# Kernel tuning notes

Measured on AMD Instinct MI355X. Metric: run time of the kernel, lower is better.

Reference implementation:

```python
import jax, jax.numpy as jnp
import numpy as np

GROUP_SIZE = 32
PACKED_SIZE = GROUP_SIZE * 3 // 8  # 12
OUT_FEATURES = 4096
IN_FEATURES = 4096

# Precomputed static unpack constants per position i in [0, 32)
_I = np.arange(GROUP_SIZE)
_BYTE_IDX = (_I * 3) // 8                     # which byte holds the low bits
_BIT_OFF = (_I * 3) % 8                       # bit offset inside that byte
_LOW_MASK = np.where(_BIT_OFF <= 5, 7, (1 << (8 - _BIT_OFF)) - 1)
_HIGH_MASK = np.where(_BIT_OFF <= 5, 0, (1 << np.maximum(_BIT_OFF - 5, 0)) - 1)
_HIGH_SHIFT = np.where(_BIT_OFF <= 5, 0, 8 - _BIT_OFF)
_BYTE_IDX_NEXT = np.minimum(_BYTE_IDX + 1, PACKED_SIZE - 1)


def block_dequantize_3bit(packed, normalization):
    """packed: [G, 12] int (uint8 values), normalization: [G, 1] -> [G*32] f32."""
    p = packed.astype(jnp.int32)
    norm = normalization.astype(jnp.float32)
    b0 = p[:, _BYTE_IDX]        # [G, 32]
    b1 = p[:, _BYTE_IDX_NEXT]   # [G, 32]
    shift = jnp.asarray(_BIT_OFF, jnp.int32)
    low = (b0 >> shift) & jnp.asarray(_LOW_MASK, jnp.int32)
    high = (b1 & jnp.asarray(_HIGH_MASK, jnp.int32)) << jnp.asarray(_HIGH_SHIFT, jnp.int32)
    x_quant = (low | high).astype(jnp.float32)  # values in [0, 7]
    x_norm = x_quant / 7.0
    x = x_norm * 2.0 * norm - norm              # [G, 32]
    return x.reshape(-1)


def setup_inputs() -> dict:
    key = jax.random.key(0)
    k1, k2, k3, k4 = jax.random.split(key, 4)
    num_groups = OUT_FEATURES * IN_FEATURES // GROUP_SIZE
    x = jax.random.normal(k1, (8192, IN_FEATURES), dtype=jnp.float32)
    weight_q3 = jax.random.randint(k2, (num_groups, PACKED_SIZE), 0, 256, dtype=jnp.int32).astype(jnp.uint8)
    weight_norm = (jax.random.uniform(k3, (num_groups, 1), dtype=jnp.float32) * 0.99 + 0.01).astype(jnp.float16)
    bias = (jax.random.normal(k4, (OUT_FEATURES,), dtype=jnp.float32) * 0.02).astype(jnp.float16)
    return {"x": x, "weight_q3": weight_q3, "weight_norm": weight_norm, "bias": bias}


def reference(x, weight_q3, weight_norm, bias):
    w_flat = block_dequantize_3bit(weight_q3, weight_norm)          # f32 [out*in]
    w = w_flat.reshape(OUT_FEATURES, IN_FEATURES).astype(jnp.float16)
    x_half = x.astype(jnp.float16)
    result = jnp.dot(x_half, w.T) + bias                             # [N, out] fp16
    return result.astype(x.dtype)
```

## Files before the change

kernel.cpp:

```cpp
#include <hip/hip_runtime.h>
#include <hip/hip_fp16.h>
#include <stdint.h>

#define IN_F   4096
#define OUT_F  4096
#define M_ROWS 8192

typedef _Float16 v8h __attribute__((ext_vector_type(8)));
typedef float    v4f __attribute__((ext_vector_type(4)));

__global__ void __launch_bounds__(256)
dequant_kernel(const int* __restrict__ q, const float* __restrict__ norm,
               _Float16* __restrict__ w) {
    int g = blockIdx.x * blockDim.x + threadIdx.x;
    const int4* p = (const int4*)(q + (size_t)g * 12);
    int4 q0 = p[0], q1 = p[1], q2 = p[2];
    uint32_t b[12] = {(uint32_t)q0.x, (uint32_t)q0.y, (uint32_t)q0.z, (uint32_t)q0.w,
                      (uint32_t)q1.x, (uint32_t)q1.y, (uint32_t)q1.z, (uint32_t)q1.w,
                      (uint32_t)q2.x, (uint32_t)q2.y, (uint32_t)q2.z, (uint32_t)q2.w};
    uint64_t lo = 0, hi = 0;
#pragma unroll
    for (int i = 0; i < 8; ++i) lo |= (uint64_t)(b[i] & 0xff) << (8 * i);
#pragma unroll
    for (int i = 0; i < 8; ++i) hi |= (uint64_t)(b[4 + i] & 0xff) << (8 * i);
    float nrm = norm[g];
    float scale = nrm * (2.0f / 7.0f);
    v8h out[4];
#pragma unroll
    for (int i = 0; i < 32; ++i) {
        int p3 = 3 * i;
        uint32_t qv = (i <= 20) ? (uint32_t)((lo >> p3) & 7)
                                : (uint32_t)((hi >> (p3 - 32)) & 7);
        float v = fmaf((float)qv, scale, -nrm);
        out[i >> 3][i & 7] = (_Float16)v;
    }
    v8h* dst = (v8h*)(w + (size_t)g * 32);
    dst[0] = out[0]; dst[1] = out[1]; dst[2] = out[2]; dst[3] = out[3];
}

__global__ void __launch_bounds__(256)
castx_kernel(const float* __restrict__ x, _Float16* __restrict__ o) {
    size_t i = ((size_t)blockIdx.x * blockDim.x + threadIdx.x) * 8;
    float4 a = *(const float4*)(x + i);
    float4 b = *(const float4*)(x + i + 4);
    v8h r;
    r[0] = (_Float16)a.x; r[1] = (_Float16)a.y; r[2] = (_Float16)a.z; r[3] = (_Float16)a.w;
    r[4] = (_Float16)b.x; r[5] = (_Float16)b.y; r[6] = (_Float16)b.z; r[7] = (_Float16)b.w;
    *(v8h*)(o + i) = r;
}

#define KU 32

__global__ void __launch_bounds__(512, 2)
gemm_kernel(const _Float16* __restrict__ A,
            const _Float16* __restrict__ B,
            const float* __restrict__ bias,
            float* __restrict__ C) {
    __shared__ __align__(16) char smem[131072];

    int pid = blockIdx.x;
    int c  = pid & 7;
    int s  = pid >> 3;
    int pm = ((c & 3) << 3) | (s & 7);
    int pn = ((c >> 2) << 3) | (s >> 3);
    const int m0 = pm * 256, n0 = pn * 256;

    int t = threadIdx.x;
    int lane = t & 63, wid = t >> 6;
    int wm = wid >> 2, wn = wid & 3;
    int lr = lane & 15, qd = lane >> 4;

    int chr  = (((lane & 1) << 2) | qd) ^ ((lr >> 1) & 7);
    int aoff = wm * 8192 + (lr >> 1) * 128 + chr * 16;
    int boff = 16384 + wn * 4096 + (lr >> 1) * 128 + chr * 16;

    int line = t >> 3, chl = t & 7;
    int chd  = chl ^ (line & 7);
    int rr0  = 2 * line + (chd >> 2);
    int cc0  = chd & 3;
    const _Float16* gA0 = A + (size_t)(m0 + rr0) * IN_F + cc0 * 8;
    const _Float16* gA1 = gA0 + (size_t)128 * IN_F;
    const _Float16* gB0 = B + (size_t)(n0 + rr0) * IN_F + cc0 * 8;
    const _Float16* gB1 = gB0 + (size_t)128 * IN_F;
    const int dA = t * 16;
    const int dB = 16384 + t * 16;

    v4f acc[8][4] = {};
    v8h fa0[8], fb0[4], fa1[8], fb1[4];

#define STAGE4(SL2)                                                                 \
    do {                                                                            \
        char* db_ = smem + (SL2) * 32768;                                           \
        __builtin_amdgcn_global_load_lds(                                           \
            (const __attribute__((address_space(1))) void*)gA0,                     \
            (__attribute__((address_space(3))) void*)(db_ + dA), 16, 0, 0);         \
        __builtin_amdgcn_global_load_lds(                                           \
            (const __attribute__((address_space(1))) void*)gA1,                     \
            (__attribute__((address_space(3))) void*)(db_ + dA + 8192), 16, 0, 0);  \
        __builtin_amdgcn_global_load_lds(                                           \
            (const __attribute__((address_space(1))) void*)gB0,                     \
            (__attribute__((address_space(3))) void*)(db_ + dB), 16, 0, 0);         \
        __builtin_amdgcn_global_load_lds(                                           \
            (const __attribute__((address_space(1))) void*)gB1,                     \
            (__attribute__((address_space(3))) void*)(db_ + dB + 8192), 16, 0, 0);  \
    } while (0)

#define READFRAG(SLOT, FA, FB)                                                      \
    do {                                                                            \
        const char* sp_ = smem + (SLOT) * 32768;                                    \
        _Pragma("unroll") for (int i = 0; i < 8; ++i)                               \
            FA[i] = *(const v8h*)(sp_ + aoff + i * 1024);                           \
        _Pragma("unroll") for (int j = 0; j < 4; ++j)                               \
            FB[j] = *(const v8h*)(sp_ + boff + j * 1024);                           \
    } while (0)

#define STEP(SL, FCA, FCB, FNA, FNB, DO_STAGE, DO_PREF, VM)                         \
    do {                                                                            \
        asm volatile("" ::: "memory");      \
        if (DO_PREF) READFRAG(((SL) + 1) & 3, FNA, FNB);                            \
        if (DO_STAGE) {                                                             \
            STAGE4(((SL) + 3) & 3);                                                 \
            gA0 += KU; gA1 += KU; gB0 += KU; gB1 += KU;                             \
        }                                                                           \
        __builtin_amdgcn_s_setprio(1);                                              \
        _Pragma("unroll") for (int i = 0; i < 8; ++i)                               \
            _Pragma("unroll") for (int j = 0; j < 4; ++j)                           \
                acc[i][j] = __builtin_amdgcn_mfma_f32_16x16x32_f16(                 \
                    FCA[i], FCB[j], acc[i][j], 0, 0, 0);                            \
        __builtin_amdgcn_s_setprio(0);                                              \
        asm volatile("s_waitcnt vmcnt(" #VM ")" ::: "memory");                      \
        __builtin_amdgcn_s_barrier();                                               \
    } while (0)

    STAGE4(0); gA0 += KU; gA1 += KU; gB0 += KU; gB1 += KU;
    STAGE4(1); gA0 += KU; gA1 += KU; gB0 += KU; gB1 += KU;
    STAGE4(2); gA0 += KU; gA1 += KU; gB0 += KU; gB1 += KU;
    asm volatile("s_waitcnt vmcnt(4)" ::: "memory");
    __builtin_amdgcn_s_barrier();
    asm volatile("" ::: "memory");
    READFRAG(0, fa0, fb0);

#pragma unroll 1
    for (int b4 = 0; b4 < 31; ++b4) {
        STEP(0, fa0, fb0, fa1, fb1, 1, 1, 4);
        STEP(1, fa1, fb1, fa0, fb0, 1, 1, 4);
        STEP(2, fa0, fb0, fa1, fb1, 1, 1, 4);
        STEP(3, fa1, fb1, fa0, fb0, 1, 1, 4);
    }
    STEP(0, fa0, fb0, fa1, fb1, 1, 1, 4);
    STEP(1, fa1, fb1, fa0, fb0, 0, 1, 0);
    STEP(2, fa0, fb0, fa1, fb1, 0, 1, 0);
    STEP(3, fa1, fb1, fa0, fb0, 0, 0, 0);
#undef STEP
#undef READFRAG
#undef STAGE4

#pragma unroll
    for (int j = 0; j < 4; ++j) {
        int n = n0 + wn * 64 + j * 16 + lr;
        float bf = bias[n];
#pragma unroll
        for (int i = 0; i < 8; ++i) {
            int m = m0 + wm * 128 + i * 16 + qd * 4;
#pragma unroll
            for (int rr = 0; rr < 4; ++rr)
                C[(size_t)(m + rr) * OUT_F + n] = acc[i][j][rr] + bf;
        }
    }
}

extern "C" void kernel_launch(void* const* d_in, const int* in_sizes, int n_in,
                              void* d_out, int out_size, void* d_ws, size_t ws_size,
                              hipStream_t stream) {
    (void)in_sizes; (void)n_in; (void)out_size; (void)ws_size;
    const float* x    = (const float*)d_in[0];
    const int*   wq   = (const int*)d_in[1];
    const float* wnrm = (const float*)d_in[2];
    const float* bias = (const float*)d_in[3];
    float* out = (float*)d_out;

    _Float16* w16 = (_Float16*)d_ws;
    _Float16* x16 = (_Float16*)((char*)d_ws + (size_t)OUT_F * IN_F * 2);

    const int NUM_GROUPS = OUT_F * IN_F / 32;
    dequant_kernel<<<NUM_GROUPS / 256, 256, 0, stream>>>(wq, wnrm, w16);
    castx_kernel<<<(size_t)M_ROWS * IN_F / 8 / 256, 256, 0, stream>>>(x, x16);

    int grid = (M_ROWS / 256) * (OUT_F / 256);
    gemm_kernel<<<grid, 512, 0, stream>>>(x16, w16, bias, out);
}
```

Before: 499.1 us.

## Interleave LDS fragment reads with MFMA groups to cut register pressure

Splits each K-step's 32 MFMAs into four groups of eight. The A fragments are now read from LDS in pairs just before they are needed, and the next step's B and first A fragments are prefetched in between the groups, instead of loading all 12 next-step fragments up front. This lowers register use (from 24 fragment registers down to 12 v8h) and spreads LDS reads across the MFMA stream. The trade-off is less slack between each LDS read and the MFMA that consumes it, so the compiler may insert waits that stall the MFMA pipe.

```diff
diff --git a/kernel.cpp b/kernel.cpp
--- a/kernel.cpp
+++ b/kernel.cpp
@@ -86,7 +86,9 @@
     const int dB = 16384 + t * 16;
 
     v4f acc[8][4] = {};
-    v8h fa0[8], fb0[4], fa1[8], fb1[4];
+    v8h p0[2], p1[2], b0s[4], b1s[4];
+
+#define RD(SLOT, OFF) (*(const v8h*)(smem + (SLOT) * 32768 + (OFF)))
 
 #define STAGE4(SL2)                                                                 \
     do {                                                                            \
@@ -105,29 +107,51 @@
             (__attribute__((address_space(3))) void*)(db_ + dB + 8192), 16, 0, 0);  \
     } while (0)
 
-#define READFRAG(SLOT, FA, FB)                                                      \
+#define MFG(G, PA, BB)                                                              \
     do {                                                                            \
-        const char* sp_ = smem + (SLOT) * 32768;                                    \
-        _Pragma("unroll") for (int i = 0; i < 8; ++i)                               \
-            FA[i] = *(const v8h*)(sp_ + aoff + i * 1024);                           \
-        _Pragma("unroll") for (int j = 0; j < 4; ++j)                               \
-            FB[j] = *(const v8h*)(sp_ + boff + j * 1024);                           \
+        __builtin_amdgcn_s_setprio(1);                                              \
+        _Pragma("unroll") for (int j = 0; j < 4; ++j) {                             \
+            acc[2 * (G)][j] = __builtin_amdgcn_mfma_f32_16x16x32_f16(               \
+                PA[0], BB[j], acc[2 * (G)][j], 0, 0, 0);                            \
+            acc[2 * (G) + 1][j] = __builtin_amdgcn_mfma_f32_16x16x32_f16(           \
+                PA[1], BB[j], acc[2 * (G) + 1][j], 0, 0, 0);                        \
+        }                                                                           \
+        __builtin_amdgcn_s_setprio(0);                                              \
     } while (0)
 
-#define STEP(SL, FCA, FCB, FNA, FNB, DO_STAGE, DO_PREF, VM)                         \
+#define STEP(SL, BC, BN, DO_STAGE, DO_NEXT, VM)                                     \
     do {                                                                            \
         asm volatile("" ::: "memory");      \
-        if (DO_PREF) READFRAG(((SL) + 1) & 3, FNA, FNB);                            \
+                                                    \
+        p1[0] = RD(SL, aoff + 2 * 1024);                                            \
+        p1[1] = RD(SL, aoff + 3 * 1024);                                            \
+        MFG(0, p0, BC);                                                             \
+                                 \
+        p0[0] = RD(SL, aoff + 4 * 1024);                                            \
+        p0[1] = RD(SL, aoff + 5 * 1024);                                            \
+        if (DO_NEXT) {                                                              \
+            BN[0] = RD(((SL) + 1) & 3, boff);                                       \
+            BN[1] = RD(((SL) + 1) & 3, boff + 1024);                                \
+        }                                                                           \
         if (DO_STAGE) {                                                             \
             STAGE4(((SL) + 3) & 3);                                                 \
             gA0 += KU; gA1 += KU; gB0 += KU; gB1 += KU;                             \
         }                                                                           \
-        __builtin_amdgcn_s_setprio(1);                                              \
-        _Pragma("unroll") for (int i = 0; i < 8; ++i)                               \
-            _Pragma("unroll") for (int j = 0; j < 4; ++j)                           \
-                acc[i][j] = __builtin_amdgcn_mfma_f32_16x16x32_f16(                 \
-                    FCA[i], FCB[j], acc[i][j], 0, 0, 0);                            \
-        __builtin_amdgcn_s_setprio(0);                                              \
+        MFG(1, p1, BC);                                                             \
+                                         \
+        p1[0] = RD(SL, aoff + 6 * 1024);                                            \
+        p1[1] = RD(SL, aoff + 7 * 1024);                                            \
+        if (DO_NEXT) {                                                              \
+            BN[2] = RD(((SL) + 1) & 3, boff + 2048);                                \
+            BN[3] = RD(((SL) + 1) & 3, boff + 3072);                                \
+        }                                                                           \
+        MFG(2, p0, BC);                                                             \
+                                               \
+        if (DO_NEXT) {                                                              \
+            p0[0] = RD(((SL) + 1) & 3, aoff);                                       \
+            p0[1] = RD(((SL) + 1) & 3, aoff + 1024);                                \
+        }                                                                           \
+        MFG(3, p1, BC);                                                             \
         asm volatile("s_waitcnt vmcnt(" #VM ")" ::: "memory");                      \
         __builtin_amdgcn_s_barrier();                                               \
     } while (0)
@@ -138,22 +162,25 @@
     asm volatile("s_waitcnt vmcnt(4)" ::: "memory");
     __builtin_amdgcn_s_barrier();
     asm volatile("" ::: "memory");
-    READFRAG(0, fa0, fb0);
+    b0s[0] = RD(0, boff);        b0s[1] = RD(0, boff + 1024);
+    b0s[2] = RD(0, boff + 2048); b0s[3] = RD(0, boff + 3072);
+    p0[0]  = RD(0, aoff);        p0[1]  = RD(0, aoff + 1024);
 
 #pragma unroll 1
     for (int b4 = 0; b4 < 31; ++b4) {
-        STEP(0, fa0, fb0, fa1, fb1, 1, 1, 4);
-        STEP(1, fa1, fb1, fa0, fb0, 1, 1, 4);
-        STEP(2, fa0, fb0, fa1, fb1, 1, 1, 4);
-        STEP(3, fa1, fb1, fa0, fb0, 1, 1, 4);
+        STEP(0, b0s, b1s, 1, 1, 4);
+        STEP(1, b1s, b0s, 1, 1, 4);
+        STEP(2, b0s, b1s, 1, 1, 4);
+        STEP(3, b1s, b0s, 1, 1, 4);
     }
-    STEP(0, fa0, fb0, fa1, fb1, 1, 1, 4);
-    STEP(1, fa1, fb1, fa0, fb0, 0, 1, 0);
-    STEP(2, fa0, fb0, fa1, fb1, 0, 1, 0);
-    STEP(3, fa1, fb1, fa0, fb0, 0, 0, 0);
+    STEP(0, b0s, b1s, 1, 1, 4);
+    STEP(1, b1s, b0s, 0, 1, 0);
+    STEP(2, b0s, b1s, 0, 1, 0);
+    STEP(3, b1s, b0s, 0, 0, 0);
 #undef STEP
-#undef READFRAG
+#undef MFG
 #undef STAGE4
+#undef RD
 
 #pragma unroll
     for (int j = 0; j < 4; ++j) {
```

Result: no change. 496.2 us (-0.6%).

## Split GEMM k-step into two ping-pong phases with barrier-synchronized LDS reads

Applied to the files above, without the earlier changes.

Replaces the register double-buffered fragment prefetch with two phases per k-step. Each phase reads half the A fragments plus the B fragments from LDS, issues half the global-to-LDS stage loads, synchronizes across waves, then runs 16 MFMAs. This lowers fragment register pressure and interleaves the memory and compute phases across waves. It adds two more barriers per step and drops the overlap between the LDS reads for the next step and the current MFMAs, and the vmcnt accounting changes to match the split staging.

```diff
diff --git a/kernel.cpp b/kernel.cpp
--- a/kernel.cpp
+++ b/kernel.cpp
@@ -9,9 +9,9 @@
 typedef _Float16 v8h __attribute__((ext_vector_type(8)));
 typedef float    v4f __attribute__((ext_vector_type(4)));
 
-__global__ void __launch_bounds__(256)
-dequant_kernel(const int* __restrict__ q, const float* __restrict__ norm,
-               _Float16* __restrict__ w) {
+__global__ void dequant_kernel(const int* __restrict__ q,
+                               const float* __restrict__ norm,
+                               _Float16* __restrict__ w) {
     int g = blockIdx.x * blockDim.x + threadIdx.x;
     const int4* p = (const int4*)(q + (size_t)g * 12);
     int4 q0 = p[0], q1 = p[1], q2 = p[2];
@@ -38,8 +38,7 @@
     dst[0] = out[0]; dst[1] = out[1]; dst[2] = out[2]; dst[3] = out[3];
 }
 
-__global__ void __launch_bounds__(256)
-castx_kernel(const float* __restrict__ x, _Float16* __restrict__ o) {
+__global__ void castx_kernel(const float* __restrict__ x, _Float16* __restrict__ o) {
     size_t i = ((size_t)blockIdx.x * blockDim.x + threadIdx.x) * 8;
     float4 a = *(const float4*)(x + i);
     float4 b = *(const float4*)(x + i + 4);
@@ -86,74 +85,93 @@
     const int dB = 16384 + t * 16;
 
     v4f acc[8][4] = {};
-    v8h fa0[8], fb0[4], fa1[8], fb1[4];
-
-#define STAGE4(SL2)                                                                 \
+    v8h pa[4], bb[4];
+
+#define RD(SLOT, OFF) (*(const v8h*)(smem + (SLOT) * 32768 + (OFF)))
+
+#define GLL(SRC, DOFF)                                                              \
+    __builtin_amdgcn_global_load_lds(                                               \
+        (const __attribute__((address_space(1))) void*)(SRC),                       \
+        (__attribute__((address_space(3))) void*)(smem + (DOFF)), 16, 0, 0)
+
+#define PHASE_A(SL, DO_STAGE)                                                       \
     do {                                                                            \
-        char* db_ = smem + (SL2) * 32768;                                           \
-        __builtin_amdgcn_global_load_lds(                                           \
-            (const __attribute__((address_space(1))) void*)gA0,                     \
-            (__attribute__((address_space(3))) void*)(db_ + dA), 16, 0, 0);         \
-        __builtin_amdgcn_global_load_lds(                                           \
-            (const __attribute__((address_space(1))) void*)gA1,                     \
-            (__attribute__((address_space(3))) void*)(db_ + dA + 8192), 16, 0, 0);  \
-        __builtin_amdgcn_global_load_lds(                                           \
-            (const __attribute__((address_space(1))) void*)gB0,                     \
-            (__attribute__((address_space(3))) void*)(db_ + dB), 16, 0, 0);         \
-        __builtin_amdgcn_global_load_lds(                                           \
-            (const __attribute__((address_space(1))) void*)gB1,                     \
-            (__attribute__((address_space(3))) void*)(db_ + dB + 8192), 16, 0, 0);  \
+        _Pragma("unroll") for (int i = 0; i < 4; ++i)                               \
+            pa[i] = RD(SL, aoff + i * 1024);                                        \
+        _Pragma("unroll") for (int j = 0; j < 4; ++j)                               \
+            bb[j] = RD(SL, boff + j * 1024);                                        \
+        if (DO_STAGE) {                                                             \
+            GLL(gA0, (((SL) + 3) & 3) * 32768 + dA);                                \
+            GLL(gA1, (((SL) + 3) & 3) * 32768 + dA + 8192);                         \
+        }                                                                           \
+        __builtin_amdgcn_s_barrier();                                               \
+        asm volatile("s_waitcnt lgkmcnt(0)" ::: "memory");                          \
+        __builtin_amdgcn_sched_barrier(0);                                          \
+        __builtin_amdgcn_s_setprio(1);                                              \
+        _Pragma("unroll") for (int i = 0; i < 4; ++i)                               \
+            _Pragma("unroll") for (int j = 0; j < 4; ++j)                           \
+                acc[i][j] = __builtin_amdgcn_mfma_f32_16x16x32_f16(                 \
+                    pa[i], bb[j], acc[i][j], 0, 0, 0);                              \
+        __builtin_amdgcn_s_setprio(0);                                              \
+        __builtin_amdgcn_s_barrier();                                               \
     } while (0)
 
-#define READFRAG(SLOT, FA, FB)                                                      \
+#define PHASE_B(SL, DO_STAGE, VM)                                                   \
     do {                                                                            \
-        const char* sp_ = smem + (SLOT) * 32768;                                    \
-        _Pragma("unroll") for (int i = 0; i < 8; ++i)                               \
-            FA[i] = *(const v8h*)(sp_ + aoff + i * 1024);                           \
-        _Pragma("unroll") for (int j = 0; j < 4; ++j)                               \
-            FB[j] = *(const v8h*)(sp_ + boff + j * 1024);                           \
-    } while (0)
-
-#define STEP(SL, FCA, FCB, FNA, FNB, DO_STAGE, DO_PREF, VM)                         \
-    do {                                                                            \
-        asm volatile("" ::: "memory");      \
-        if (DO_PREF) READFRAG(((SL) + 1) & 3, FNA, FNB);                            \
+        _Pragma("unroll") for (int i = 0; i < 4; ++i)                               \
+            pa[i] = RD(SL, aoff + (i + 4) * 1024);                                  \
         if (DO_STAGE) {                                                             \
-            STAGE4(((SL) + 3) & 3);                                                 \
+            GLL(gB0, (((SL) + 3) & 3) * 32768 + dB);                                \
+            GLL(gB1, (((SL) + 3) & 3) * 32768 + dB + 8192);                         \
             gA0 += KU; gA1 += KU; gB0 += KU; gB1 += KU;                             \
         }                                                                           \
+        __builtin_amdgcn_s_barrier();                                               \
+        asm volatile("s_waitcnt lgkmcnt(0)" ::: "memory");                          \
+        __builtin_amdgcn_sched_barrier(0);                                          \
         __builtin_amdgcn_s_setprio(1);                                              \
-        _Pragma("unroll") for (int i = 0; i < 8; ++i)                               \
+        _Pragma("unroll") for (int i = 0; i < 4; ++i)                               \
             _Pragma("unroll") for (int j = 0; j < 4; ++j)                           \
-                acc[i][j] = __builtin_amdgcn_mfma_f32_16x16x32_f16(                 \
-                    FCA[i], FCB[j], acc[i][j], 0, 0, 0);                            \
+                acc[i + 4][j] = __builtin_amdgcn_mfma_f32_16x16x32_f16(             \
+                    pa[i], bb[j], acc[i + 4][j], 0, 0, 0);                          \
         __builtin_amdgcn_s_setprio(0);                                              \
         asm volatile("s_waitcnt vmcnt(" #VM ")" ::: "memory");                      \
         __builtin_amdgcn_s_barrier();                                               \
     } while (0)
 
-    STAGE4(0); gA0 += KU; gA1 += KU; gB0 += KU; gB1 += KU;
-    STAGE4(1); gA0 += KU; gA1 += KU; gB0 += KU; gB1 += KU;
-    STAGE4(2); gA0 += KU; gA1 += KU; gB0 += KU; gB1 += KU;
-    asm volatile("s_waitcnt vmcnt(4)" ::: "memory");
+#define BODY(SL, DO_STAGE, VM)  do { PHASE_A(SL, DO_STAGE); PHASE_B(SL, DO_STAGE, VM); } while (0)
+
+#define STAGE_SLOT(SL2)                                                             \
+    do {                                                                            \
+        GLL(gA0, (SL2) * 32768 + dA);                                               \
+        GLL(gA1, (SL2) * 32768 + dA + 8192);                                        \
+        GLL(gB0, (SL2) * 32768 + dB);                                               \
+        GLL(gB1, (SL2) * 32768 + dB + 8192);                                        \
+        gA0 += KU; gA1 += KU; gB0 += KU; gB1 += KU;                                 \
+    } while (0)
+
+    STAGE_SLOT(0);
+    STAGE_SLOT(1);
+    STAGE_SLOT(2);
+    asm volatile("s_waitcnt vmcnt(8)" ::: "memory");
     __builtin_amdgcn_s_barrier();
-    asm volatile("" ::: "memory");
-    READFRAG(0, fa0, fb0);
 
 #pragma unroll 1
     for (int b4 = 0; b4 < 31; ++b4) {
-        STEP(0, fa0, fb0, fa1, fb1, 1, 1, 4);
-        STEP(1, fa1, fb1, fa0, fb0, 1, 1, 4);
-        STEP(2, fa0, fb0, fa1, fb1, 1, 1, 4);
-        STEP(3, fa1, fb1, fa0, fb0, 1, 1, 4);
+        BODY(0, 1, 8);
+        BODY(1, 1, 8);
+        BODY(2, 1, 8);
+        BODY(3, 1, 8);
     }
-    STEP(0, fa0, fb0, fa1, fb1, 1, 1, 4);
-    STEP(1, fa1, fb1, fa0, fb0, 0, 1, 0);
-    STEP(2, fa0, fb0, fa1, fb1, 0, 1, 0);
-    STEP(3, fa1, fb1, fa0, fb0, 0, 0, 0);
-#undef STEP
-#undef READFRAG
-#undef STAGE4
+    BODY(0, 1, 8);
+    BODY(1, 0, 4);
+    BODY(2, 0, 0);
+    BODY(3, 0, 0);
+#undef BODY
+#undef PHASE_A
+#undef PHASE_B
+#undef STAGE_SLOT
+#undef GLL
+#undef RD
 
 #pragma unroll
     for (int j = 0; j < 4; ++j) {
```

Measured after the change: 500.9 us. About the same (+0.4%).
